# Optimization experiments

Measured on AMD Instinct MI355X. Metric: run time of the kernel, lower is better.

The kernel has to match this reference:

```python
import jax, jax.numpy as jnp
import numpy as np


def _conv1x1_relu(x, w, b):
    # x: [B,C,H,W], w: [O,C], b: [O] -> relu(1x1 conv) [B,O,H,W]
    y = jnp.einsum('oc,bchw->bohw', w, x) + b[None, :, None, None]
    return jax.nn.relu(y)


def setup_inputs() -> dict:
    key = jax.random.key(0)
    ks = jax.random.split(key, 9)
    B, C, H, W = 16, 128, 256, 64
    s = 1.0 / np.sqrt(C)
    return {
        'rep': jax.random.normal(ks[0], (B, C, H, W), jnp.float32),
        'wq': jax.random.normal(ks[1], (C, C), jnp.float32) * s,
        'bq': jax.random.normal(ks[2], (C,), jnp.float32) * 0.02,
        'wk': jax.random.normal(ks[3], (C, C), jnp.float32) * s,
        'bk': jax.random.normal(ks[4], (C,), jnp.float32) * 0.02,
        'wv': jax.random.normal(ks[5], (C, C), jnp.float32) * s,
        'bv': jax.random.normal(ks[6], (C,), jnp.float32) * 0.02,
        'wfc': jax.random.normal(ks[7], (C, C), jnp.float32) * s,
        'bfc': jax.random.normal(ks[8], (C,), jnp.float32) * 0.02,
    }


def reference(rep, wq, bq, wk, bk, wv, bv, wfc, bfc):
    C = rep.shape[1]
    # ReLU-activated 1x1-conv Q/K/V projections, then permute to [B,W,H,C]
    q = _conv1x1_relu(rep, wq, bq).transpose(0, 3, 2, 1)  # [B,W,H,C]
    k = _conv1x1_relu(rep, wk, bk).transpose(0, 3, 2, 1)
    v = _conv1x1_relu(rep, wv, bv).transpose(0, 3, 2, 1)
    # attention over the H axis, independently per (B, W)
    attn = jnp.einsum('bwhc,bwgc->bwhg', q, k) / jnp.sqrt(jnp.asarray(C, q.dtype))
    attn = jax.nn.softmax(attn, axis=-1)  # [B,W,H,H]
    out = jnp.einsum('bwhg,bwgc->bwhc', attn, v)  # [B,W,H,C]
    # back to NCHW, final ReLU 1x1 conv
    out = out.transpose(0, 3, 2, 1)  # [B,C,H,W]
    return _conv1x1_relu(out, wfc, bfc)
```

## Files before the change

kernel.cpp:

```cpp
#include <hip/hip_runtime.h>


typedef __attribute__((ext_vector_type(8))) short short8;
typedef __attribute__((ext_vector_type(4))) float f32x4;
typedef __attribute__((ext_vector_type(4))) int int4v;

#define MFMA16(acc, a, b) (acc) = __builtin_amdgcn_mfma_f32_16x16x32_bf16((a), (b), (acc), 0, 0, 0)

__device__ __forceinline__ unsigned short f2b(float f) {
  unsigned u = __builtin_bit_cast(unsigned, f);
  u = (u + 0x7fffu + ((u >> 16) & 1u)) >> 16;
  return (unsigned short)u;
}

__device__ __forceinline__ unsigned adr_s(int r, int c) {
  return (unsigned)(((r << 8) + (c << 1)) ^ ((r & 7) << 4));
}
__device__ __forceinline__ unsigned adr_q(int r, int c) {
  return (unsigned)(((r << 8) + (c << 1)) ^ (((r ^ (r >> 3)) & 7) << 4));
}
__device__ __forceinline__ unsigned adr_vt(int c, int g) {
  unsigned blk = (unsigned)(((g >> 3) ^ (c & 7) ^ ((c >> 3) & 7)) & 31);
  return (unsigned)((c << 9) + (blk << 4) + ((g & 7) << 1));
}
__device__ __forceinline__ unsigned ps_adr(int r, int c) {
  return (unsigned)(((r << 7) + (c << 1)) ^ (((r ^ (r >> 3)) & 7) << 4));
}

__device__ __forceinline__ short8 ldsf(const char* p, unsigned off) {
  return *(const short8*)(p + off);
}

__global__ __launch_bounds__(256) void k0_wcvt(
    const float* __restrict__ wq, const float* __restrict__ wk,
    const float* __restrict__ wv, const float* __restrict__ wfc,
    unsigned short* __restrict__ wb)
{
  int i = blockIdx.x * 256 + threadIdx.x;
  int mat = i >> 12, off = (i & 4095) * 4;
  const float* src = (mat == 0) ? wq : (mat == 1) ? wk : (mat == 2) ? wv : wfc;
  float4 v = *(const float4*)(src + off);
  uint2 u;
  u.x = (unsigned)f2b(v.x) | ((unsigned)f2b(v.y) << 16);
  u.y = (unsigned)f2b(v.z) | ((unsigned)f2b(v.w) << 16);
  *(uint2*)(wb + mat * 16384 + off) = u;
}


__device__ __forceinline__ void k1_one(const unsigned short* wmat, const float* bias,
    unsigned short* dst, const char* XS, char* WS,
    int brel, int n0, int wvid, int l, int l16, int g4) {
  const int strip = wvid * 16;
  short8 wf[4];
#pragma unroll
  for (int kk = 0; kk < 4; ++kk)
    wf[kk] = *(const short8*)(wmat + (strip + l16) * 128 + kk * 32 + g4 * 8);
  float bv4[4];
#pragma unroll
  for (int r = 0; r < 4; ++r) bv4[r] = bias[strip + g4 * 4 + r];

  f32x4 acc[8];
#pragma unroll
  for (int nt = 0; nt < 8; ++nt) acc[nt] = (f32x4){0.f, 0.f, 0.f, 0.f};
#pragma unroll
  for (int nt = 0; nt < 8; ++nt) {
#pragma unroll
    for (int kk = 0; kk < 4; ++kk) {
      short8 xb = ldsf(XS, adr_q(nt * 16 + l16, kk * 32 + g4 * 8));
      MFMA16(acc[nt], wf[kk], xb);
    }
  }
#pragma unroll
  for (int qt = 0; qt < 4; ++qt) {
    __syncthreads();
#pragma unroll
    for (int nt2 = 0; nt2 < 2; ++nt2) {
      int nt = qt * 2 + nt2;
      float y0 = fmaxf(acc[nt][0] + bv4[0], 0.f);
      float y1 = fmaxf(acc[nt][1] + bv4[1], 0.f);
      float y2 = fmaxf(acc[nt][2] + bv4[2], 0.f);
      float y3 = fmaxf(acc[nt][3] + bv4[3], 0.f);
      uint2 u;
      u.x = (unsigned)f2b(y0) | ((unsigned)f2b(y1) << 16);
      u.y = (unsigned)f2b(y2) | ((unsigned)f2b(y3) << 16);
      int row = nt2 * 16 + l16;
      unsigned cb = (unsigned)(wvid * 32 + g4 * 8);
      *(uint2*)(WS + (unsigned)(row << 8) + (cb ^ ((unsigned)(row & 7) << 4))) = u;
    }
    __syncthreads();
#pragma unroll
    for (int it = 0; it < 4; ++it) {
      int row = it * 8 + wvid;
      unsigned u = *(const unsigned*)(WS + (unsigned)(row << 8) +
                                     (((unsigned)(l << 2)) ^ ((unsigned)(row & 7) << 4)));
      int n = n0 + qt * 32 + row;
      int h = n >> 6, w = n & 63;
      ((unsigned*)dst)[(size_t)((brel * 64 + w) * 256 + h) * 64 + l] = u;
    }
  }
}

__global__ __launch_bounds__(512, 4) void k1_qkv(
    const float* __restrict__ rep, const unsigned short* __restrict__ wb,
    const float* __restrict__ bq, const float* __restrict__ bk,
    const float* __restrict__ bv,
    unsigned short* __restrict__ qo, unsigned short* __restrict__ ko,
    unsigned short* __restrict__ vo, int b0)
{
  extern __shared__ char smem[];
  char* XS = smem;
  char* WS = smem + (32 << 10);

  const int t = threadIdx.x;
  const int wvid = t >> 6, l = t & 63, l16 = l & 15, g4 = l >> 4;
  const int brel = blockIdx.x >> 7;
  const int n0 = (blockIdx.x & 127) * 128;
  const int b = b0 + brel;

#pragma unroll
  for (int it = 0; it < 8; ++it) {
    int i = it * 512 + t;
    int c = i >> 5, j4 = i & 31;
    float4 xv = *(const float4*)(rep + (size_t)(b * 128 + c) * 16384 + n0 + j4 * 4);
    float vv[4] = {xv.x, xv.y, xv.z, xv.w};
#pragma unroll
    for (int r = 0; r < 4; ++r)
      *(unsigned short*)(XS + adr_q(j4 * 4 + r, c)) = f2b(vv[r]);
  }
  __syncthreads();

  k1_one(wb,         bq, qo, XS, WS, brel, n0, wvid, l, l16, g4);
  k1_one(wb + 16384, bk, ko, XS, WS, brel, n0, wvid, l, l16, g4);
  k1_one(wb + 32768, bv, vo, XS, WS, brel, n0, wvid, l, l16, g4);
}


__global__ __launch_bounds__(512, 2) void k2_attn(
    const unsigned short* __restrict__ qws, const unsigned short* __restrict__ kws,
    const unsigned short* __restrict__ vws, unsigned short* __restrict__ aws)
{
  extern __shared__ char smem[];
  char* KS  = smem;
  char* VTS = smem + (64 << 10);

  const int t = threadIdx.x;
  const int wvid = t >> 6, l = t & 63, l16 = l & 15, g4 = l >> 4;
  char* PS = smem + (128 << 10) + (wvid << 11);

  const int brel = blockIdx.x >> 6;
  const int w = blockIdx.x & 63;
  const size_t wbase = (size_t)((brel * 64 + w)) * 256;

  const int hb0 = wvid * 32;
  const int hb1 = wvid * 32 + 16;

  short8 qa0[4], qa1[4];
#pragma unroll
  for (int kk = 0; kk < 4; ++kk) {
    qa0[kk] = *(const short8*)(qws + (wbase + hb0 + l16) * 128 + kk * 32 + g4 * 8);
    qa1[kk] = *(const short8*)(qws + (wbase + hb1 + l16) * 128 + kk * 32 + g4 * 8);
  }

#pragma unroll
  for (int it = 0; it < 8; ++it) {
    int i = it * 512 + t;
    int g = i >> 4, c16 = i & 15;
    int gp = (g & ~31) | ((g & 4) << 2) | ((g >> 1) & 12) | (g & 3);
    short8 kv = *(const short8*)(kws + (wbase + g) * 128 + c16 * 8);
    *(short8*)(KS + adr_s(gp, c16 * 8)) = kv;
  }
#pragma unroll
  for (int it = 0; it < 8; ++it) {
    int i = it * 512 + t;
    int g = i >> 4, c16 = i & 15;
    short8 vv = *(const short8*)(vws + (wbase + g) * 128 + c16 * 8);
#pragma unroll
    for (int j = 0; j < 8; ++j)
      *(unsigned short*)(VTS + adr_vt(c16 * 8 + j, g)) = (unsigned short)vv[j];
  }
  __syncthreads();

  const float SCL2 = 0.08838834764831845f * 1.4426950408889634f;

  f32x4 sc0[16], sc1[16];
#pragma unroll
  for (int gt = 0; gt < 16; ++gt) {
    f32x4 a0 = {0.f, 0.f, 0.f, 0.f};
    f32x4 a1 = {0.f, 0.f, 0.f, 0.f};
#pragma unroll
    for (int kk = 0; kk < 4; ++kk) {
      short8 kb = ldsf(KS, adr_s(gt * 16 + l16, kk * 32 + g4 * 8));
      MFMA16(a0, kb, qa0[kk]);
      MFMA16(a1, kb, qa1[kk]);
    }
    sc0[gt] = a0;
    sc1[gt] = a1;
  }

  unsigned pk0a[16], pk1a[16];
  {
    float mm = fmaxf(fmaxf(sc0[0][0], sc0[0][1]), fmaxf(sc0[0][2], sc0[0][3]));
#pragma unroll
    for (int gt = 1; gt < 16; ++gt) {
      float m4 = fmaxf(fmaxf(sc0[gt][0], sc0[gt][1]), fmaxf(sc0[gt][2], sc0[gt][3]));
      mm = fmaxf(mm, m4);
    }
    mm = fmaxf(mm, __shfl_xor(mm, 16, 64));
    mm = fmaxf(mm, __shfl_xor(mm, 32, 64));
    const float mneg = -mm * SCL2;
    float s = 0.f;
#pragma unroll
    for (int gt = 0; gt < 16; ++gt) {
#pragma unroll
      for (int r = 0; r < 4; ++r) {
        float p = exp2f(fmaf(sc0[gt][r], SCL2, mneg));
        sc0[gt][r] = p;
        s += p;
      }
    }
    s += __shfl_xor(s, 16, 64);
    s += __shfl_xor(s, 32, 64);
    const float rcp = 1.0f / s;
#pragma unroll
    for (int gt = 0; gt < 16; ++gt) {
      pk0a[gt] = (unsigned)f2b(sc0[gt][0] * rcp) | ((unsigned)f2b(sc0[gt][1] * rcp) << 16);
      pk1a[gt] = (unsigned)f2b(sc0[gt][2] * rcp) | ((unsigned)f2b(sc0[gt][3] * rcp) << 16);
    }
  }
  unsigned pk0b[16], pk1b[16];
  {
    float mm = fmaxf(fmaxf(sc1[0][0], sc1[0][1]), fmaxf(sc1[0][2], sc1[0][3]));
#pragma unroll
    for (int gt = 1; gt < 16; ++gt) {
      float m4 = fmaxf(fmaxf(sc1[gt][0], sc1[gt][1]), fmaxf(sc1[gt][2], sc1[gt][3]));
      mm = fmaxf(mm, m4);
    }
    mm = fmaxf(mm, __shfl_xor(mm, 16, 64));
    mm = fmaxf(mm, __shfl_xor(mm, 32, 64));
    const float mneg = -mm * SCL2;
    float s = 0.f;
#pragma unroll
    for (int gt = 0; gt < 16; ++gt) {
#pragma unroll
      for (int r = 0; r < 4; ++r) {
        float p = exp2f(fmaf(sc1[gt][r], SCL2, mneg));
        sc1[gt][r] = p;
        s += p;
      }
    }
    s += __shfl_xor(s, 16, 64);
    s += __shfl_xor(s, 32, 64);
    const float rcp = 1.0f / s;
#pragma unroll
    for (int gt = 0; gt < 16; ++gt) {
      pk0b[gt] = (unsigned)f2b(sc1[gt][0] * rcp) | ((unsigned)f2b(sc1[gt][1] * rcp) << 16);
      pk1b[gt] = (unsigned)f2b(sc1[gt][2] * rcp) | ((unsigned)f2b(sc1[gt][3] * rcp) << 16);
    }
  }

  f32x4 oacc0[8], oacc1[8];
#pragma unroll
  for (int nt = 0; nt < 8; ++nt) {
    oacc0[nt] = (f32x4){0.f, 0.f, 0.f, 0.f};
    oacc1[nt] = (f32x4){0.f, 0.f, 0.f, 0.f};
  }
#pragma unroll
  for (int kks = 0; kks < 8; ++kks) {
    int4v pv0 = {(int)pk0a[2 * kks], (int)pk1a[2 * kks],
                 (int)pk0a[2 * kks + 1], (int)pk1a[2 * kks + 1]};
    int4v pv1 = {(int)pk0b[2 * kks], (int)pk1b[2 * kks],
                 (int)pk0b[2 * kks + 1], (int)pk1b[2 * kks + 1]};
    short8 pa0 = __builtin_bit_cast(short8, pv0);
    short8 pa1 = __builtin_bit_cast(short8, pv1);
#pragma unroll
    for (int nt = 0; nt < 8; ++nt) {
      short8 vb = ldsf(VTS, adr_vt(nt * 16 + l16, kks * 32 + g4 * 8));
      MFMA16(oacc0[nt], pa0, vb);
      MFMA16(oacc1[nt], pa1, vb);
    }
  }

#pragma unroll
  for (int m = 0; m < 2; ++m) {
    const int hb = (m == 0) ? hb0 : hb1;
#pragma unroll
    for (int ch = 0; ch < 2; ++ch) {
#pragma unroll
      for (int nt4 = 0; nt4 < 4; ++nt4) {
        int nt = ch * 4 + nt4;
        f32x4 ov = (m == 0) ? oacc0[nt] : oacc1[nt];
#pragma unroll
        for (int r = 0; r < 4; ++r)
          *(unsigned short*)(PS + ps_adr(g4 * 4 + r, nt4 * 16 + l16)) = f2b(ov[r]);
      }
#pragma unroll
      for (int it = 0; it < 8; ++it) {
        int row = it * 2 + (l >> 5);
        int cd  = l & 31;
        unsigned base = (unsigned)(row << 7) +
            (((unsigned)(cd << 2)) ^ (((unsigned)((row ^ (row >> 3)) & 7)) << 4));
        unsigned lo = *(const unsigned short*)(PS + base);
        unsigned hi = *(const unsigned short*)(PS + base + 2);
        ((unsigned*)aws)[(wbase + hb + row) * 64 + ch * 32 + cd] = lo | (hi << 16);
      }
    }
  }
}


__global__ __launch_bounds__(512, 4) void k3_conv(
    const unsigned short* __restrict__ aws, const unsigned short* __restrict__ wb,
    const float* __restrict__ bfc, float* __restrict__ out, int b0)
{
  extern __shared__ char smem[];
  char* AS = smem;

  const int t = threadIdx.x;
  const int wvid = t >> 6, l = t & 63, l16 = l & 15, g4 = l >> 4;
  (void)l;
  const int brel = blockIdx.x >> 6;
  const int n0 = (blockIdx.x & 63) * 256;
  const int b = b0 + brel;

#pragma unroll
  for (int it = 0; it < 8; ++it) {
    int i = it * 512 + t;
    int nn = i >> 4, c16 = i & 15;
    int n = n0 + nn;
    int h = n >> 6, w = n & 63;
    short8 av = *(const short8*)(aws + ((size_t)((brel * 64 + w) * 256 + h)) * 128 + c16 * 8);
    *(short8*)(AS + adr_s(nn, c16 * 8)) = av;
  }
  __syncthreads();

  const int strip = wvid * 16;
  const unsigned short* wfcb = wb + 3 * 16384;
  short8 wf[4];
#pragma unroll
  for (int kk = 0; kk < 4; ++kk)
    wf[kk] = *(const short8*)(wfcb + (strip + l16) * 128 + kk * 32 + g4 * 8);
  float bv4[4];
#pragma unroll
  for (int r = 0; r < 4; ++r) bv4[r] = bfc[strip + g4 * 4 + r];

#pragma unroll
  for (int nt = 0; nt < 16; ++nt) {
    f32x4 acc = {0.f, 0.f, 0.f, 0.f};
#pragma unroll
    for (int kk = 0; kk < 4; ++kk) {
      short8 ab = ldsf(AS, adr_s(nt * 16 + l16, kk * 32 + g4 * 8));
      MFMA16(acc, wf[kk], ab);
    }
#pragma unroll
    for (int r = 0; r < 4; ++r) {
      int o = strip + g4 * 4 + r;
      out[(size_t)(b * 128 + o) * 16384 + n0 + nt * 16 + l16] = fmaxf(acc[r] + bv4[r], 0.f);
    }
  }
}

extern "C" void kernel_launch(void* const* d_in, const int* in_sizes, int n_in,
                              void* d_out, int out_size, void* d_ws, size_t ws_size,
                              hipStream_t stream) {
  const float* rep = (const float*)d_in[0];
  const float* wq  = (const float*)d_in[1];
  const float* bq  = (const float*)d_in[2];
  const float* wk  = (const float*)d_in[3];
  const float* bk  = (const float*)d_in[4];
  const float* wv  = (const float*)d_in[5];
  const float* bv  = (const float*)d_in[6];
  const float* wfc = (const float*)d_in[7];
  const float* bfc = (const float*)d_in[8];
  float* out = (float*)d_out;
  (void)in_sizes; (void)n_in; (void)out_size;

  hipFuncSetAttribute((const void*)k1_qkv,  hipFuncAttributeMaxDynamicSharedMemorySize, 40 * 1024);
  hipFuncSetAttribute((const void*)k2_attn, hipFuncAttributeMaxDynamicSharedMemorySize, 144 * 1024);
  hipFuncSetAttribute((const void*)k3_conv, hipFuncAttributeMaxDynamicSharedMemorySize, 64 * 1024);

  const size_t wb_bytes = 4 * 16384 * 2;
  const size_t per_b = (size_t)16384 * 128 * 2;
  if (ws_size < wb_bytes + 4 * per_b) return;
  size_t nb_max = (ws_size - wb_bytes) / (4 * per_b);
  int nb = (int)(nb_max < 16 ? nb_max : 16);

  char* ws = (char*)d_ws;
  unsigned short* qws = (unsigned short*)(ws);
  unsigned short* kws = (unsigned short*)(ws + (size_t)nb * per_b);
  unsigned short* vws = (unsigned short*)(ws + (size_t)nb * per_b * 2);
  unsigned short* aws = (unsigned short*)(ws + (size_t)nb * per_b * 3);
  unsigned short* wb  = (unsigned short*)(ws + (size_t)nb * per_b * 4);

  k0_wcvt<<<dim3(64), dim3(256), 0, stream>>>(wq, wk, wv, wfc, wb);

  for (int b0 = 0; b0 < 16; b0 += nb) {
    int nbc = (16 - b0) < nb ? (16 - b0) : nb;
    k1_qkv<<<dim3(nbc * 128), dim3(512), 40 * 1024, stream>>>(
        rep, wb, bq, bk, bv, qws, kws, vws, b0);
    k2_attn<<<dim3(nbc * 64), dim3(512), 144 * 1024, stream>>>(qws, kws, vws, aws);
    k3_conv<<<dim3(nbc * 64), dim3(512), 64 * 1024, stream>>>(aws, wb, bfc, out, b0);
  }
}
```

Measured before the change: 229.3 us.

## Restructure QKV projection so each wave owns a pixel strip, removing block barriers

The QKV 1x1-conv kernel previously split output channels across waves and shared a block-wide X tile, which needed a __syncthreads pair per output quarter for the transpose staging. Now each wave loads its own 16-pixel strip of X into private LDS, keeps the X fragments in registers, loops over all 128 output channels streaming weight fragments from global memory, and transposes through a private per-wave LDS buffer. This removes all block-level barriers. In exchange, each wave reads the full weight matrices (more global/L2 traffic), MFMA work per wave becomes a serial dependent loop, and LDS per block grows to 64KB, which may reduce occupancy.

After: 352.3 us. +53.6%, slower.

```diff
diff --git a/kernel.cpp b/kernel.cpp
--- a/kernel.cpp
+++ b/kernel.cpp
@@ -16,15 +16,18 @@
 __device__ __forceinline__ unsigned adr_s(int r, int c) {
   return (unsigned)(((r << 8) + (c << 1)) ^ ((r & 7) << 4));
 }
-__device__ __forceinline__ unsigned adr_q(int r, int c) {
-  return (unsigned)(((r << 8) + (c << 1)) ^ (((r ^ (r >> 3)) & 7) << 4));
-}
 __device__ __forceinline__ unsigned adr_vt(int c, int g) {
   unsigned blk = (unsigned)(((g >> 3) ^ (c & 7) ^ ((c >> 3) & 7)) & 31);
   return (unsigned)((c << 9) + (blk << 4) + ((g & 7) << 1));
 }
 __device__ __forceinline__ unsigned ps_adr(int r, int c) {
   return (unsigned)(((r << 7) + (c << 1)) ^ (((r ^ (r >> 3)) & 7) << 4));
+}
+__device__ __forceinline__ unsigned xsw_adr(int j, int c) {
+  return (unsigned)(((j << 8) + (c << 1)) ^ (((j ^ (j >> 3)) & 7) << 4));
+}
+__device__ __forceinline__ unsigned psw_adr(int row, int cbyte) {
+  return (unsigned)(((row << 8) + cbyte) ^ ((row & 7) << 4));
 }
 
 __device__ __forceinline__ short8 ldsf(const char* p, unsigned off) {
@@ -47,56 +50,39 @@
 }
 
 
-__device__ __forceinline__ void k1_one(const unsigned short* wmat, const float* bias,
-    unsigned short* dst, const char* XS, char* WS,
-    int brel, int n0, int wvid, int l, int l16, int g4) {
-  const int strip = wvid * 16;
-  short8 wf[4];
-#pragma unroll
-  for (int kk = 0; kk < 4; ++kk)
-    wf[kk] = *(const short8*)(wmat + (strip + l16) * 128 + kk * 32 + g4 * 8);
-  float bv4[4];
-#pragma unroll
-  for (int r = 0; r < 4; ++r) bv4[r] = bias[strip + g4 * 4 + r];
-
+__device__ __forceinline__ void k1_mat(const unsigned short* wmat, const float* bias,
+    unsigned short* dst, const char* XSW, char* PSW, const short8* xb,
+    int brel, int wn0, int l, int l16, int g4) {
   f32x4 acc[8];
 #pragma unroll
-  for (int nt = 0; nt < 8; ++nt) acc[nt] = (f32x4){0.f, 0.f, 0.f, 0.f};
-#pragma unroll
-  for (int nt = 0; nt < 8; ++nt) {
-#pragma unroll
-    for (int kk = 0; kk < 4; ++kk) {
-      short8 xb = ldsf(XS, adr_q(nt * 16 + l16, kk * 32 + g4 * 8));
-      MFMA16(acc[nt], wf[kk], xb);
-    }
-  }
-#pragma unroll
-  for (int qt = 0; qt < 4; ++qt) {
-    __syncthreads();
-#pragma unroll
-    for (int nt2 = 0; nt2 < 2; ++nt2) {
-      int nt = qt * 2 + nt2;
-      float y0 = fmaxf(acc[nt][0] + bv4[0], 0.f);
-      float y1 = fmaxf(acc[nt][1] + bv4[1], 0.f);
-      float y2 = fmaxf(acc[nt][2] + bv4[2], 0.f);
-      float y3 = fmaxf(acc[nt][3] + bv4[3], 0.f);
-      uint2 u;
-      u.x = (unsigned)f2b(y0) | ((unsigned)f2b(y1) << 16);
-      u.y = (unsigned)f2b(y2) | ((unsigned)f2b(y3) << 16);
-      int row = nt2 * 16 + l16;
-      unsigned cb = (unsigned)(wvid * 32 + g4 * 8);
-      *(uint2*)(WS + (unsigned)(row << 8) + (cb ^ ((unsigned)(row & 7) << 4))) = u;
-    }
-    __syncthreads();
-#pragma unroll
-    for (int it = 0; it < 4; ++it) {
-      int row = it * 8 + wvid;
-      unsigned u = *(const unsigned*)(WS + (unsigned)(row << 8) +
-                                     (((unsigned)(l << 2)) ^ ((unsigned)(row & 7) << 4)));
-      int n = n0 + qt * 32 + row;
-      int h = n >> 6, w = n & 63;
-      ((unsigned*)dst)[(size_t)((brel * 64 + w) * 256 + h) * 64 + l] = u;
-    }
+  for (int os = 0; os < 8; ++os) acc[os] = (f32x4){0.f, 0.f, 0.f, 0.f};
+
+#pragma unroll 1
+  for (int os = 0; os < 8; ++os) {
+    short8 wf[4];
+#pragma unroll
+    for (int kk = 0; kk < 4; ++kk)
+      wf[kk] = *(const short8*)(wmat + (os * 16 + l16) * 128 + kk * 32 + g4 * 8);
+    float4 b4 = *(const float4*)(bias + os * 16 + g4 * 4);
+#pragma unroll
+    for (int kk = 0; kk < 4; ++kk)
+      MFMA16(acc[os], wf[kk], xb[kk]);
+    float y0 = fmaxf(acc[os][0] + b4.x, 0.f);
+    float y1 = fmaxf(acc[os][1] + b4.y, 0.f);
+    float y2 = fmaxf(acc[os][2] + b4.z, 0.f);
+    float y3 = fmaxf(acc[os][3] + b4.w, 0.f);
+    unsigned u0 = (unsigned)f2b(y0) | ((unsigned)f2b(y1) << 16);
+    unsigned u1 = (unsigned)f2b(y2) | ((unsigned)f2b(y3) << 16);
+    unsigned cb = (unsigned)(os * 32 + g4 * 8);
+    *(unsigned*)(PSW + psw_adr(l16, cb))     = u0;
+    *(unsigned*)(PSW + psw_adr(l16, cb + 4)) = u1;
+  }
+#pragma unroll
+  for (int it = 0; it < 16; ++it) {
+    unsigned u = *(const unsigned*)(PSW + psw_adr(it, l << 2));
+    int ng = wn0 + it;
+    int h = ng >> 6, w = ng & 63;
+    ((unsigned*)dst)[(size_t)((brel * 64 + w) * 256 + h) * 64 + l] = u;
   }
 }
 
@@ -108,30 +94,34 @@
     unsigned short* __restrict__ vo, int b0)
 {
   extern __shared__ char smem[];
-  char* XS = smem;
-  char* WS = smem + (32 << 10);
-
   const int t = threadIdx.x;
   const int wvid = t >> 6, l = t & 63, l16 = l & 15, g4 = l >> 4;
+  char* XSW = smem + wvid * 8192;
+  char* PSW = XSW + 4096;
+
   const int brel = blockIdx.x >> 7;
   const int n0 = (blockIdx.x & 127) * 128;
   const int b = b0 + brel;
+  const int wn0 = n0 + wvid * 16;
 
 #pragma unroll
   for (int it = 0; it < 8; ++it) {
-    int i = it * 512 + t;
-    int c = i >> 5, j4 = i & 31;
-    float4 xv = *(const float4*)(rep + (size_t)(b * 128 + c) * 16384 + n0 + j4 * 4);
+    int c = it * 16 + (l >> 2);
+    int j4 = l & 3;
+    float4 xv = *(const float4*)(rep + (size_t)(b * 128 + c) * 16384 + wn0 + j4 * 4);
     float vv[4] = {xv.x, xv.y, xv.z, xv.w};
 #pragma unroll
     for (int r = 0; r < 4; ++r)
-      *(unsigned short*)(XS + adr_q(j4 * 4 + r, c)) = f2b(vv[r]);
-  }
-  __syncthreads();
-
-  k1_one(wb,         bq, qo, XS, WS, brel, n0, wvid, l, l16, g4);
-  k1_one(wb + 16384, bk, ko, XS, WS, brel, n0, wvid, l, l16, g4);
-  k1_one(wb + 32768, bv, vo, XS, WS, brel, n0, wvid, l, l16, g4);
+      *(unsigned short*)(XSW + xsw_adr(j4 * 4 + r, c)) = f2b(vv[r]);
+  }
+  short8 xb[4];
+#pragma unroll
+  for (int kk = 0; kk < 4; ++kk)
+    xb[kk] = ldsf(XSW, xsw_adr(l16, kk * 32 + g4 * 8));
+
+  k1_mat(wb,         bq, qo, XSW, PSW, xb, brel, wn0, l, l16, g4);
+  k1_mat(wb + 16384, bk, ko, XSW, PSW, xb, brel, wn0, l, l16, g4);
+  k1_mat(wb + 32768, bv, vo, XSW, PSW, xb, brel, wn0, l, l16, g4);
 }
 
 
@@ -374,7 +364,7 @@
   float* out = (float*)d_out;
   (void)in_sizes; (void)n_in; (void)out_size;
 
-  hipFuncSetAttribute((const void*)k1_qkv,  hipFuncAttributeMaxDynamicSharedMemorySize, 40 * 1024);
+  hipFuncSetAttribute((const void*)k1_qkv,  hipFuncAttributeMaxDynamicSharedMemorySize, 64 * 1024);
   hipFuncSetAttribute((const void*)k2_attn, hipFuncAttributeMaxDynamicSharedMemorySize, 144 * 1024);
   hipFuncSetAttribute((const void*)k3_conv, hipFuncAttributeMaxDynamicSharedMemorySize, 64 * 1024);
 
@@ -395,7 +385,7 @@
 
   for (int b0 = 0; b0 < 16; b0 += nb) {
     int nbc = (16 - b0) < nb ? (16 - b0) : nb;
-    k1_qkv<<<dim3(nbc * 128), dim3(512), 40 * 1024, stream>>>(
+    k1_qkv<<<dim3(nbc * 128), dim3(512), 64 * 1024, stream>>>(
         rep, wb, bq, bk, bv, qws, kws, vws, b0);
     k2_attn<<<dim3(nbc * 64), dim3(512), 144 * 1024, stream>>>(qws, kws, vws, aws);
     k3_conv<<<dim3(nbc * 64), dim3(512), 64 * 1024, stream>>>(aws, wb, bfc, out, b0);
```

## Write Q/K/V in MFMA-fragment-native layout, drop LDS transpose staging

Applied to the files above, without the earlier changes.

The QKV projection kernel now writes each MFMA accumulator fragment directly to global memory in a custom tiled layout (sidx), instead of staging through shared memory with barriers to transpose into [B,W,H,C] rows. The attention kernel reads Q/K/V through a matching gather helper built from two 8-byte loads. This removes the LDS round trip and eight barriers per projection and cuts k1's shared memory. In exchange, k1 stores and k2 loads become strided 8-byte accesses, which may coalesce less well than the previous contiguous row accesses.

Result: slower. 520.9 us (+127.1%).

```diff
diff --git a/kernel.cpp b/kernel.cpp
--- a/kernel.cpp
+++ b/kernel.cpp
@@ -13,6 +13,11 @@
   return (unsigned short)u;
 }
 
+__device__ __forceinline__ unsigned sidx(int n, int o2) {
+  return ((unsigned)(((n >> 4) * 8 + (o2 >> 3)) * 64 + ((o2 >> 1) & 3) * 16 + (n & 15)) << 1)
+         + (unsigned)(o2 & 1);
+}
+
 __device__ __forceinline__ unsigned adr_s(int r, int c) {
   return (unsigned)(((r << 8) + (c << 1)) ^ ((r & 7) << 4));
 }
@@ -29,6 +34,12 @@
 
 __device__ __forceinline__ short8 ldsf(const char* p, unsigned off) {
   return *(const short8*)(p + off);
+}
+__device__ __forceinline__ short8 sld(const unsigned* base, int n, int c16) {
+  uint2 ua = *(const uint2*)(base + sidx(n, c16 * 4));
+  uint2 ub = *(const uint2*)(base + sidx(n, c16 * 4 + 2));
+  int4v v = {(int)ua.x, (int)ua.y, (int)ub.x, (int)ub.y};
+  return __builtin_bit_cast(short8, v);
 }
 
 __global__ __launch_bounds__(256) void k0_wcvt(
@@ -48,55 +59,31 @@
 
 
 __device__ __forceinline__ void k1_one(const unsigned short* wmat, const float* bias,
-    unsigned short* dst, const char* XS, char* WS,
-    int brel, int n0, int wvid, int l, int l16, int g4) {
+    unsigned* dst, const char* XS,
+    int n0, int wvid, int l16, int g4) {
   const int strip = wvid * 16;
   short8 wf[4];
 #pragma unroll
   for (int kk = 0; kk < 4; ++kk)
     wf[kk] = *(const short8*)(wmat + (strip + l16) * 128 + kk * 32 + g4 * 8);
-  float bv4[4];
-#pragma unroll
-  for (int r = 0; r < 4; ++r) bv4[r] = bias[strip + g4 * 4 + r];
-
-  f32x4 acc[8];
-#pragma unroll
-  for (int nt = 0; nt < 8; ++nt) acc[nt] = (f32x4){0.f, 0.f, 0.f, 0.f};
+  float4 b4 = *(const float4*)(bias + strip + g4 * 4);
+
 #pragma unroll
   for (int nt = 0; nt < 8; ++nt) {
+    f32x4 acc = {0.f, 0.f, 0.f, 0.f};
 #pragma unroll
     for (int kk = 0; kk < 4; ++kk) {
       short8 xb = ldsf(XS, adr_q(nt * 16 + l16, kk * 32 + g4 * 8));
-      MFMA16(acc[nt], wf[kk], xb);
-    }
-  }
-#pragma unroll
-  for (int qt = 0; qt < 4; ++qt) {
-    __syncthreads();
-#pragma unroll
-    for (int nt2 = 0; nt2 < 2; ++nt2) {
-      int nt = qt * 2 + nt2;
-      float y0 = fmaxf(acc[nt][0] + bv4[0], 0.f);
-      float y1 = fmaxf(acc[nt][1] + bv4[1], 0.f);
-      float y2 = fmaxf(acc[nt][2] + bv4[2], 0.f);
-      float y3 = fmaxf(acc[nt][3] + bv4[3], 0.f);
-      uint2 u;
-      u.x = (unsigned)f2b(y0) | ((unsigned)f2b(y1) << 16);
-      u.y = (unsigned)f2b(y2) | ((unsigned)f2b(y3) << 16);
-      int row = nt2 * 16 + l16;
-      unsigned cb = (unsigned)(wvid * 32 + g4 * 8);
-      *(uint2*)(WS + (unsigned)(row << 8) + (cb ^ ((unsigned)(row & 7) << 4))) = u;
-    }
-    __syncthreads();
-#pragma unroll
-    for (int it = 0; it < 4; ++it) {
-      int row = it * 8 + wvid;
-      unsigned u = *(const unsigned*)(WS + (unsigned)(row << 8) +
-                                     (((unsigned)(l << 2)) ^ ((unsigned)(row & 7) << 4)));
-      int n = n0 + qt * 32 + row;
-      int h = n >> 6, w = n & 63;
-      ((unsigned*)dst)[(size_t)((brel * 64 + w) * 256 + h) * 64 + l] = u;
-    }
+      MFMA16(acc, wf[kk], xb);
+    }
+    float y0 = fmaxf(acc[0] + b4.x, 0.f);
+    float y1 = fmaxf(acc[1] + b4.y, 0.f);
+    float y2 = fmaxf(acc[2] + b4.z, 0.f);
+    float y3 = fmaxf(acc[3] + b4.w, 0.f);
+    uint2 u;
+    u.x = (unsigned)f2b(y0) | ((unsigned)f2b(y1) << 16);
+    u.y = (unsigned)f2b(y2) | ((unsigned)f2b(y3) << 16);
+    *(uint2*)(dst + sidx(n0 + nt * 16 + l16, wvid * 8 + g4 * 2)) = u;
   }
 }
 
@@ -104,18 +91,19 @@
     const float* __restrict__ rep, const unsigned short* __restrict__ wb,
     const float* __restrict__ bq, const float* __restrict__ bk,
     const float* __restrict__ bv,
-    unsigned short* __restrict__ qo, unsigned short* __restrict__ ko,
-    unsigned short* __restrict__ vo, int b0)
+    unsigned* __restrict__ qo, unsigned* __restrict__ ko,
+    unsigned* __restrict__ vo, int b0)
 {
   extern __shared__ char smem[];
   char* XS = smem;
-  char* WS = smem + (32 << 10);
 
   const int t = threadIdx.x;
   const int wvid = t >> 6, l = t & 63, l16 = l & 15, g4 = l >> 4;
+  (void)l;
   const int brel = blockIdx.x >> 7;
   const int n0 = (blockIdx.x & 127) * 128;
   const int b = b0 + brel;
+  const unsigned boff = (unsigned)brel * 1048576u;
 
 #pragma unroll
   for (int it = 0; it < 8; ++it) {
@@ -129,15 +117,15 @@
   }
   __syncthreads();
 
-  k1_one(wb,         bq, qo, XS, WS, brel, n0, wvid, l, l16, g4);
-  k1_one(wb + 16384, bk, ko, XS, WS, brel, n0, wvid, l, l16, g4);
-  k1_one(wb + 32768, bv, vo, XS, WS, brel, n0, wvid, l, l16, g4);
+  k1_one(wb,         bq, qo + boff, XS, n0, wvid, l16, g4);
+  k1_one(wb + 16384, bk, ko + boff, XS, n0, wvid, l16, g4);
+  k1_one(wb + 32768, bv, vo + boff, XS, n0, wvid, l16, g4);
 }
 
 
 __global__ __launch_bounds__(512, 2) void k2_attn(
-    const unsigned short* __restrict__ qws, const unsigned short* __restrict__ kws,
-    const unsigned short* __restrict__ vws, unsigned short* __restrict__ aws)
+    const unsigned* __restrict__ qws, const unsigned* __restrict__ kws,
+    const unsigned* __restrict__ vws, unsigned short* __restrict__ aws)
 {
   extern __shared__ char smem[];
   char* KS  = smem;
@@ -149,7 +137,11 @@
 
   const int brel = blockIdx.x >> 6;
   const int w = blockIdx.x & 63;
-  const size_t wbase = (size_t)((brel * 64 + w)) * 256;
+  const unsigned boff = (unsigned)brel * 1048576u;
+  const unsigned* qp = qws + boff;
+  const unsigned* kp = kws + boff;
+  const unsigned* vp = vws + boff;
+  const size_t wbase = (size_t)(brel * 64 + w) * 256;
 
   const int hb0 = wvid * 32;
   const int hb1 = wvid * 32 + 16;
@@ -157,8 +149,8 @@
   short8 qa0[4], qa1[4];
 #pragma unroll
   for (int kk = 0; kk < 4; ++kk) {
-    qa0[kk] = *(const short8*)(qws + (wbase + hb0 + l16) * 128 + kk * 32 + g4 * 8);
-    qa1[kk] = *(const short8*)(qws + (wbase + hb1 + l16) * 128 + kk * 32 + g4 * 8);
+    qa0[kk] = sld(qp, (hb0 + l16) * 64 + w, kk * 4 + g4);
+    qa1[kk] = sld(qp, (hb1 + l16) * 64 + w, kk * 4 + g4);
   }
 
 #pragma unroll
@@ -166,14 +158,14 @@
     int i = it * 512 + t;
     int g = i >> 4, c16 = i & 15;
     int gp = (g & ~31) | ((g & 4) << 2) | ((g >> 1) & 12) | (g & 3);
-    short8 kv = *(const short8*)(kws + (wbase + g) * 128 + c16 * 8);
+    short8 kv = sld(kp, g * 64 + w, c16);
     *(short8*)(KS + adr_s(gp, c16 * 8)) = kv;
   }
 #pragma unroll
   for (int it = 0; it < 8; ++it) {
     int i = it * 512 + t;
     int g = i >> 4, c16 = i & 15;
-    short8 vv = *(const short8*)(vws + (wbase + g) * 128 + c16 * 8);
+    short8 vv = sld(vp, g * 64 + w, c16);
 #pragma unroll
     for (int j = 0; j < 8; ++j)
       *(unsigned short*)(VTS + adr_vt(c16 * 8 + j, g)) = (unsigned short)vv[j];
@@ -374,7 +366,7 @@
   float* out = (float*)d_out;
   (void)in_sizes; (void)n_in; (void)out_size;
 
-  hipFuncSetAttribute((const void*)k1_qkv,  hipFuncAttributeMaxDynamicSharedMemorySize, 40 * 1024);
+  hipFuncSetAttribute((const void*)k1_qkv,  hipFuncAttributeMaxDynamicSharedMemorySize, 32 * 1024);
   hipFuncSetAttribute((const void*)k2_attn, hipFuncAttributeMaxDynamicSharedMemorySize, 144 * 1024);
   hipFuncSetAttribute((const void*)k3_conv, hipFuncAttributeMaxDynamicSharedMemorySize, 64 * 1024);
 
@@ -385,9 +377,9 @@
   int nb = (int)(nb_max < 16 ? nb_max : 16);
 
   char* ws = (char*)d_ws;
-  unsigned short* qws = (unsigned short*)(ws);
-  unsigned short* kws = (unsigned short*)(ws + (size_t)nb * per_b);
-  unsigned short* vws = (unsigned short*)(ws + (size_t)nb * per_b * 2);
+  unsigned* qws = (unsigned*)(ws);
+  unsigned* kws = (unsigned*)(ws + (size_t)nb * per_b);
+  unsigned* vws = (unsigned*)(ws + (size_t)nb * per_b * 2);
   unsigned short* aws = (unsigned short*)(ws + (size_t)nb * per_b * 3);
   unsigned short* wb  = (unsigned short*)(ws + (size_t)nb * per_b * 4);
 
@@ -395,7 +387,7 @@
 
   for (int b0 = 0; b0 < 16; b0 += nb) {
     int nbc = (16 - b0) < nb ? (16 - b0) : nb;
-    k1_qkv<<<dim3(nbc * 128), dim3(512), 40 * 1024, stream>>>(
+    k1_qkv<<<dim3(nbc * 128), dim3(512), 32 * 1024, stream>>>(
         rep, wb, bq, bk, bv, qws, kws, vws, b0);
     k2_attn<<<dim3(nbc * 64), dim3(512), 144 * 1024, stream>>>(qws, kws, vws, aws);
     k3_conv<<<dim3(nbc * 64), dim3(512), 64 * 1024, stream>>>(aws, wb, bfc, out, b0);
```
